# Performance work log

Hardware: AMD Instinct MI355X
Metric: run time of the kernel (lower is better)

## Reference

```python
import jax, jax.numpy as jnp
import numpy as np

DIM = 1024
NUM_HEADS = 16
HEAD_DIM = DIM // NUM_HEADS
CHUNK = 128
SCALE = HEAD_DIM ** -0.5
RMS_EPS_BIT = 1.1920929e-07  # torch.finfo(float32).eps (nn.RMSNorm default)
RMS_EPS_OUT = 1e-6


def activation_quant(x):
    scale = 127.0 / jnp.clip(jnp.max(jnp.abs(x), axis=-1, keepdims=True), 1e-5)
    return jnp.clip(jnp.round(x * scale), -128, 127) / scale


def weight_quant(w):
    scale = 1.0 / jnp.clip(jnp.mean(jnp.abs(w)), 1e-5)
    return jnp.clip(jnp.round(w * scale), -1, 1) / scale


def bitlinear(x, w, b, norm_w):
    xn = x * jax.lax.rsqrt(jnp.mean(x * x, axis=-1, keepdims=True) + RMS_EPS_BIT) * norm_w
    xq = xn + jax.lax.stop_gradient(activation_quant(xn) - xn)
    wq = w + jax.lax.stop_gradient(weight_quant(w) - w)
    return xq @ wq.T + b


def rms_norm(x, w):
    return x * jax.lax.rsqrt(jnp.mean(x * x, axis=-1, keepdims=True) + RMS_EPS_OUT) * w


def apply_rope(x, cos, sin):
    # x: [B,N,H,D]; cos/sin: [N, D//2]
    B, N, H, D = x.shape
    cos_e = jnp.repeat(cos[:N], 2, axis=-1)[None, :, None, :]  # [1,N,1,D]
    sin_e = jnp.repeat(sin[:N], 2, axis=-1)[None, :, None, :]
    xh = x.reshape(B, N, H, D // 2, 2)
    x_rot = jnp.stack([-xh[..., 1], xh[..., 0]], axis=-1).reshape(B, N, H, D)
    return x * cos_e + x_rot * sin_e


def setup_inputs() -> dict:
    key = jax.random.key(0)
    ks = jax.random.split(key, 8)
    B, N = 2, 8192
    return {
        "x": jax.random.normal(ks[0], (B, N, DIM), jnp.float32),
        "cos": jax.random.uniform(ks[1], (N, HEAD_DIM // 2), jnp.float32),
        "sin": jax.random.uniform(ks[2], (N, HEAD_DIM // 2), jnp.float32),
        "qkv_w": jax.random.normal(ks[3], (3 * DIM, DIM), jnp.float32) * 0.02,
        "qkv_b": jnp.zeros((3 * DIM,), jnp.float32),
        "qkv_nw": jnp.ones((DIM,), jnp.float32),
        "proj_w": jax.random.normal(ks[4], (DIM, DIM), jnp.float32) * 0.02,
        "proj_b": jnp.zeros((DIM,), jnp.float32),
        "proj_nw": jnp.ones((DIM,), jnp.float32),
        "norm_w": jnp.ones((DIM,), jnp.float32),
    }


def lightning_attention(x, cos, sin, qkv_w, qkv_b, qkv_nw, proj_w, proj_b, proj_nw, norm_w):
    B, N, C = x.shape
    qkv = bitlinear(x, qkv_w, qkv_b, qkv_nw).reshape(B, N, 3, NUM_HEADS, HEAD_DIM)
    q, k, v = qkv[:, :, 0], qkv[:, :, 1], qkv[:, :, 2]
    q = apply_rope(q, cos, sin)
    k = apply_rope(k, cos, sin)
    # N chosen as a multiple of CHUNK (pad_len == 0)
    T = N // CHUNK
    # [T, B, chunk, H, Dh]
    qc = jnp.moveaxis(q.reshape(B, T, CHUNK, NUM_HEADS, HEAD_DIM), 1, 0)
    kc = jnp.moveaxis(k.reshape(B, T, CHUNK, NUM_HEADS, HEAD_DIM), 1, 0)
    vc = jnp.moveaxis(v.reshape(B, T, CHUNK, NUM_HEADS, HEAD_DIM), 1, 0)
    causal = jnp.tril(jnp.ones((CHUNK, CHUNK), bool))
    neg_inf = jnp.finfo(x.dtype).min

    def step(kv_state, chunk):
        q_t, k_t, v_t = chunk  # each [B, chunk, H, Dh]
        scores = jnp.einsum('bqhd,bkhd->bhqk', q_t, k_t) * SCALE
        scores = jnp.where(causal, scores, neg_inf)
        attn = jax.nn.softmax(scores, axis=-1)
        o_intra = jnp.einsum('bhqk,bkhd->bqhd', attn, v_t)
        o_inter = jnp.einsum('bqhd,bhde->bqhe', q_t, kv_state)
        kv_new = kv_state + jnp.einsum('bkhd,bkhe->bhde', k_t, v_t)
        return kv_new, o_intra + o_inter

    kv0 = jnp.zeros((B, NUM_HEADS, HEAD_DIM, HEAD_DIM), x.dtype)
    _, out = jax.lax.scan(step, kv0, (qc, kc, vc))  # out: [T,B,chunk,H,Dh]
    out = jnp.moveaxis(out, 0, 1).reshape(B, N, C)
    return bitlinear(rms_norm(out, norm_w), proj_w, proj_b, proj_nw)


def reference(x, cos, sin, qkv_w, qkv_b, qkv_nw, proj_w, proj_b, proj_nw, norm_w):
    return lightning_attention(x, cos, sin, qkv_w, qkv_b, qkv_nw, proj_w, proj_b, proj_nw, norm_w)
```

## Files before the change

kernel.cpp:

```cpp
#include <hip/hip_runtime.h>


typedef unsigned short USH;
typedef __attribute__((ext_vector_type(8))) short short8;
typedef __attribute__((ext_vector_type(4))) float f32x4;
typedef __attribute__((ext_vector_type(4))) USH us4;

__device__ __forceinline__ float b2f(USH u) { return __uint_as_float(((unsigned)u) << 16); }
__device__ __forceinline__ USH f2b(float f) {
    unsigned u = __float_as_uint(f);
    u += 0x7fffu + ((u >> 16) & 1u);
    return (USH)(u >> 16);
}
__device__ __forceinline__ f32x4 mfma16(short8 a, short8 b, f32x4 c) {
    return __builtin_amdgcn_mfma_f32_16x16x32_bf16(a, b, c, 0, 0, 0);
}
__device__ __forceinline__ void gload_lds16(const void* g, void* l) {
    __builtin_amdgcn_global_load_lds(
        (const __attribute__((address_space(1))) unsigned*)g,
        (__attribute__((address_space(3))) unsigned*)l, 16, 0, 0);
}

__device__ __forceinline__ float blk_sum(float v, float* red) {
#pragma unroll
    for (int o = 32; o; o >>= 1) v += __shfl_xor(v, o);
    __syncthreads();
    if ((threadIdx.x & 63) == 0) red[threadIdx.x >> 6] = v;
    __syncthreads();
    return red[0] + red[1] + red[2] + red[3];
}
__device__ __forceinline__ float blk_max(float v, float* red) {
#pragma unroll
    for (int o = 32; o; o >>= 1) v = fmaxf(v, __shfl_xor(v, o));
    __syncthreads();
    if ((threadIdx.x & 63) == 0) red[threadIdx.x >> 6] = v;
    __syncthreads();
    return fmaxf(fmaxf(red[0], red[1]), fmaxf(red[2], red[3]));
}

__global__ __launch_bounds__(256) void k_wabs(const float* __restrict__ qw,
                                              const float* __restrict__ pw,
                                              float* __restrict__ partials) {
    __shared__ float red[4];
    int which = blockIdx.y;
    const float4* p = (const float4*)(which ? pw : qw);
    int n4 = which ? (1024 * 1024 / 4) : (3072 * 1024 / 4);
    float s = 0.f;
    for (int i = blockIdx.x * 256 + threadIdx.x; i < n4; i += 256 * 256) {
        float4 v = p[i];
        s += fabsf(v.x) + fabsf(v.y) + fabsf(v.z) + fabsf(v.w);
    }
#pragma unroll
    for (int o = 32; o; o >>= 1) s += __shfl_xor(s, o);
    if ((threadIdx.x & 63) == 0) red[threadIdx.x >> 6] = s;
    __syncthreads();
    if (threadIdx.x == 0)
        partials[which * 256 + blockIdx.x] = red[0] + red[1] + red[2] + red[3];
}

__global__ __launch_bounds__(256) void k_wsum(const float* __restrict__ partials,
                                              float* __restrict__ sums) {
    __shared__ double red[4];
    int which = blockIdx.x;
    double v = (double)partials[which * 256 + threadIdx.x];
#pragma unroll
    for (int o = 32; o; o >>= 1) v += __shfl_xor(v, o);
    if ((threadIdx.x & 63) == 0) red[threadIdx.x >> 6] = v;
    __syncthreads();
    if (threadIdx.x == 0)
        sums[which] = (float)(red[0] + red[1] + red[2] + red[3]);
}

__global__ __launch_bounds__(256) void k_wquant(const float* __restrict__ qw,
                                                const float* __restrict__ pw,
                                                const float* __restrict__ sums,
                                                USH* __restrict__ wqk, USH* __restrict__ wqp) {
    int id = blockIdx.x * 256 + threadIdx.x;
    float4 v; USH* dst; float sc;
    if (id < 786432) {
        v = ((const float4*)qw)[id];
        sc = 1.f / fmaxf(sums[0] * (1.f / 3145728.f), 1e-5f);
        dst = wqk + (size_t)id * 4;
    } else {
        int j = id - 786432;
        v = ((const float4*)pw)[j];
        sc = 1.f / fmaxf(sums[1] * (1.f / 1048576.f), 1e-5f);
        dst = wqp + (size_t)j * 4;
    }
    us4 o;
    o.x = f2b(fminf(fmaxf(rintf(v.x * sc), -1.f), 1.f));
    o.y = f2b(fminf(fmaxf(rintf(v.y * sc), -1.f), 1.f));
    o.z = f2b(fminf(fmaxf(rintf(v.z * sc), -1.f), 1.f));
    o.w = f2b(fminf(fmaxf(rintf(v.w * sc), -1.f), 1.f));
    *(us4*)dst = o;
}

__global__ __launch_bounds__(256) void k_actq(const float* __restrict__ x,
                                              const float* __restrict__ nw,
                                              USH* __restrict__ xq, float* __restrict__ inva) {
    __shared__ float red[4];
    int row = blockIdx.x, tid = threadIdx.x;
    float4 v = ((const float4*)(x + (size_t)row * 1024))[tid];
    float4 w = ((const float4*)nw)[tid];
    float ss = v.x * v.x + v.y * v.y + v.z * v.z + v.w * v.w;
    ss = blk_sum(ss, red);
    float r1 = rsqrtf(ss * (1.f / 1024.f) + 1.1920929e-07f);
    float x0 = v.x * r1 * w.x, x1 = v.y * r1 * w.y, x2 = v.z * r1 * w.z, x3 = v.w * r1 * w.w;
    float am = fmaxf(fmaxf(fabsf(x0), fabsf(x1)), fmaxf(fabsf(x2), fabsf(x3)));
    am = blk_max(am, red);
    float amc = fmaxf(am, 1e-5f);
    float sc = 127.f / amc;
    us4 o;
    o.x = f2b(fminf(fmaxf(rintf(x0 * sc), -128.f), 127.f));
    o.y = f2b(fminf(fmaxf(rintf(x1 * sc), -128.f), 127.f));
    o.z = f2b(fminf(fmaxf(rintf(x2 * sc), -128.f), 127.f));
    o.w = f2b(fminf(fmaxf(rintf(x3 * sc), -128.f), 127.f));
    *(us4*)(xq + (size_t)row * 1024 + tid * 4) = o;
    if (tid == 0) inva[row] = amc * (1.f / 127.f);
}

__global__ __launch_bounds__(256) void k_norm2q(const USH* __restrict__ oat,
                                                const float* __restrict__ nw,
                                                const float* __restrict__ pnw,
                                                USH* __restrict__ xq, float* __restrict__ inva) {
    __shared__ float red[4];
    int row = blockIdx.x, tid = threadIdx.x;
    us4 ov = *(const us4*)(oat + (size_t)row * 1024 + tid * 4);
    float o0 = b2f(ov.x), o1 = b2f(ov.y), o2 = b2f(ov.z), o3 = b2f(ov.w);
    float4 w = ((const float4*)nw)[tid];
    float4 pw = ((const float4*)pnw)[tid];
    float ss1 = blk_sum(o0 * o0 + o1 * o1 + o2 * o2 + o3 * o3, red);
    float r1 = rsqrtf(ss1 * (1.f / 1024.f) + 1e-6f);
    float y0 = o0 * r1 * w.x, y1 = o1 * r1 * w.y, y2 = o2 * r1 * w.z, y3 = o3 * r1 * w.w;
    float ss2 = blk_sum(y0 * y0 + y1 * y1 + y2 * y2 + y3 * y3, red);
    float r2 = rsqrtf(ss2 * (1.f / 1024.f) + 1.1920929e-07f);
    float z0 = y0 * r2 * pw.x, z1 = y1 * r2 * pw.y, z2 = y2 * r2 * pw.z, z3 = y3 * r2 * pw.w;
    float am = fmaxf(fmaxf(fabsf(z0), fabsf(z1)), fmaxf(fabsf(z2), fabsf(z3)));
    am = blk_max(am, red);
    float amc = fmaxf(am, 1e-5f);
    float sc = 127.f / amc;
    us4 q;
    q.x = f2b(fminf(fmaxf(rintf(z0 * sc), -128.f), 127.f));
    q.y = f2b(fminf(fmaxf(rintf(z1 * sc), -128.f), 127.f));
    q.z = f2b(fminf(fmaxf(rintf(z2 * sc), -128.f), 127.f));
    q.w = f2b(fminf(fmaxf(rintf(z3 * sc), -128.f), 127.f));
    *(us4*)(xq + (size_t)row * 1024 + tid * 4) = q;
    if (tid == 0) inva[row] = amc * (1.f / 127.f);
}

template <bool OUT_BF16>
__global__ __launch_bounds__(512, 2) void k_gemm(const USH* __restrict__ A, const USH* __restrict__ W,
                                                 const float* __restrict__ inva,
                                                 const float* __restrict__ wsum, float wcnt,
                                                 const float* __restrict__ bias,
                                                 void* __restrict__ out, int Nn, int K) {
    __shared__ __align__(16) USH lds[3 * 16384];
    const int tid = threadIdx.x;
    const int wv = tid >> 6, lane = tid & 63, quad = lane >> 4, lid = lane & 15;
    const int wr = wv >> 2, wc = wv & 3;

    const int nbn = gridDim.x;
    const int nwg = nbn * gridDim.y;
    const int bid = blockIdx.y * nbn + blockIdx.x;
    const int swb = (bid & 7) * (nwg >> 3) + (bid >> 3);
    const int bn = swb % nbn, bm = swb / nbn;

    const int T = K >> 5;

    const int r0s = wv * 16 + (lane >> 2);
    const int sw0 = (r0s & 3) ^ ((r0s >> 2) & 1);
    const int c0s = ((lane & 3) ^ sw0) * 8;
    const USH* ag0 = A + (size_t)(bm * 256 + r0s) * K + c0s;
    const USH* wg0 = W + (size_t)(bn * 256 + r0s) * K + c0s;
    const size_t J1 = (size_t)128 * K;

    const int sq = quad ^ ((lid & 3) ^ ((lid >> 2) & 1));
    const int arow = (wr * 128 + lid) * 32 + sq * 8;
    const int brow = (wc * 64 + lid) * 32 + sq * 8;

    f32x4 acc[8][4];
#pragma unroll
    for (int mt = 0; mt < 8; mt++)
#pragma unroll
        for (int nt = 0; nt < 4; nt++)
#pragma unroll
            for (int r = 0; r < 4; r++) acc[mt][nt][r] = 0.f;

#pragma unroll
    for (int t = 0; t < 3; t++) {
        USH* dst = &lds[t * 16384];
        gload_lds16(ag0 + t * 32,      &dst[wv * 512]);
        gload_lds16(ag0 + J1 + t * 32, &dst[(8 + wv) * 512]);
        gload_lds16(wg0 + t * 32,      &dst[8192 + wv * 512]);
        gload_lds16(wg0 + J1 + t * 32, &dst[8192 + (8 + wv) * 512]);
    }
    asm volatile("s_waitcnt vmcnt(8)" ::: "memory");
    __builtin_amdgcn_s_barrier();
    __builtin_amdgcn_sched_barrier(0);

    short8 afA[8], bfA[4], afB[8], bfB[4];
#pragma unroll
    for (int mt = 0; mt < 8; mt++) afA[mt] = *(const short8*)&lds[arow + mt * 512];
#pragma unroll
    for (int nt = 0; nt < 4; nt++) bfA[nt] = *(const short8*)&lds[8192 + brow + nt * 512];

#define GITER(t, afC, bfC, afN, bfN)                                              \
    do {                                                                          \
        const USH* Rd = &lds[(((t) + 1) % 3) * 16384];                            \
        USH* Sd = &lds[((t) % 3) * 16384];                                        \
        if ((t) + 2 < T) asm volatile("s_waitcnt vmcnt(4) lgkmcnt(0)" ::: "memory"); \
        else             asm volatile("s_waitcnt vmcnt(0) lgkmcnt(0)" ::: "memory"); \
        __builtin_amdgcn_s_barrier();                                             \
        __builtin_amdgcn_sched_barrier(0);                                        \
        if ((t) + 3 < T) {                                                        \
            gload_lds16(ag0 + ((t) + 3) * 32,      &Sd[wv * 512]);                \
            gload_lds16(ag0 + J1 + ((t) + 3) * 32, &Sd[(8 + wv) * 512]);          \
            gload_lds16(wg0 + ((t) + 3) * 32,      &Sd[8192 + wv * 512]);         \
            gload_lds16(wg0 + J1 + ((t) + 3) * 32, &Sd[8192 + (8 + wv) * 512]);   \
        }                                                                         \
        if ((t) + 1 < T) {                                                        \
            _Pragma("unroll")                                                     \
            for (int mt_ = 0; mt_ < 8; mt_++)                                     \
                afN[mt_] = *(const short8*)&Rd[arow + mt_ * 512];                 \
            _Pragma("unroll")                                                     \
            for (int nt_ = 0; nt_ < 4; nt_++)                                     \
                bfN[nt_] = *(const short8*)&Rd[8192 + brow + nt_ * 512];          \
        }                                                                         \
        __builtin_amdgcn_s_setprio(1);                                            \
        _Pragma("unroll")                                                         \
        for (int mt_ = 0; mt_ < 8; mt_++)                                         \
            _Pragma("unroll")                                                     \
            for (int nt_ = 0; nt_ < 4; nt_++)                                     \
                acc[mt_][nt_] = mfma16(afC[mt_], bfC[nt_], acc[mt_][nt_]);        \
        __builtin_amdgcn_s_setprio(0);                                            \
    } while (0)

    for (int tt = 0; tt < T; tt += 2) {
        GITER(tt,     afA, bfA, afB, bfB);
        GITER(tt + 1, afB, bfB, afA, bfA);
    }
#undef GITER

    float wm = fmaxf(wsum[0] * (1.f / wcnt), 1e-5f);
#pragma unroll
    for (int mt = 0; mt < 8; mt++)
#pragma unroll
        for (int r = 0; r < 4; r++) {
            int rowg = bm * 256 + wr * 128 + mt * 16 + quad * 4 + r;
            float ia = inva[rowg] * wm;
#pragma unroll
            for (int nt = 0; nt < 4; nt++) {
                int colg = bn * 256 + wc * 64 + nt * 16 + lid;
                float v = acc[mt][nt][r] * ia + bias[colg];
                if (OUT_BF16) ((USH*)out)[(size_t)rowg * Nn + colg] = f2b(v);
                else ((float*)out)[(size_t)rowg * Nn + colg] = v;
            }
        }
}

__global__ __launch_bounds__(256) void k_rope(USH* __restrict__ qkv,
                                              const float* __restrict__ cs,
                                              const float* __restrict__ sn) {
    int id = blockIdx.x * 256 + threadIdx.x;
    int rowm = id >> 8, p4 = id & 255;
    int part = p4 >> 7, pi = p4 & 127;
    int h = pi >> 3, i4 = pi & 7;
    int n = rowm & 8191;
    size_t a = (size_t)rowm * 3072 + part * 1024 + h * 64 + i4 * 8;
    short8 u = *(const short8*)(qkv + a);
    float4 c4 = *(const float4*)&cs[n * 32 + i4 * 4];
    float4 s4 = *(const float4*)&sn[n * 32 + i4 * 4];
    float c[4] = {c4.x, c4.y, c4.z, c4.w};
    float s[4] = {s4.x, s4.y, s4.z, s4.w};
    short8 y;
#pragma unroll
    for (int p = 0; p < 4; p++) {
        float x0 = b2f((USH)u[2 * p]);
        float x1 = b2f((USH)u[2 * p + 1]);
        y[2 * p]     = (short)f2b(x0 * c[p] - x1 * s[p]);
        y[2 * p + 1] = (short)f2b(x1 * c[p] + x0 * s[p]);
    }
    *(short8*)(qkv + a) = y;
}

__global__ __launch_bounds__(256) void k_attn_intra(const USH* __restrict__ qkv,
                                                    USH* __restrict__ oat,
                                                    float* __restrict__ kvc) {
    __shared__ char smem[36864 + 17408 + 17408];
    USH* qs = (USH*)smem;
    USH* kqs = qs + 128 * 72;
    USH* Ps = (USH*)smem;
    USH* vt = (USH*)(smem + 36864);
    USH* kt = (USH*)(smem + 36864 + 17408);
    int tid = threadIdx.x, wv = tid >> 6, lane = tid & 63, quad = lane >> 4, lid = lane & 15;
    int t = blockIdx.x, bh = blockIdx.y, b = bh >> 4, h = bh & 15;
    size_t base = ((size_t)(b * 8192 + t * 128)) * 3072 + h * 64;
    int r0 = tid >> 3, c0 = (tid & 7) * 8;
#pragma unroll
    for (int i = 0; i < 4; i++) {
        int r = i * 32 + r0;
        short8 qv = *(const short8*)(qkv + base + (size_t)r * 3072 + c0);
        short8 kv = *(const short8*)(qkv + base + (size_t)r * 3072 + 1024 + c0);
        short8 vv = *(const short8*)(qkv + base + (size_t)r * 3072 + 2048 + c0);
        *(short8*)&qs[r * 72 + c0] = qv;
        *(short8*)&kqs[r * 72 + c0] = kv;
        USH tmpv[8]; *(short8*)tmpv = vv;
        USH tmpk[8]; *(short8*)tmpk = kv;
#pragma unroll
        for (int j = 0; j < 8; j++) {
            vt[(c0 + j) * 136 + r] = tmpv[j];
            kt[(c0 + j) * 136 + r] = tmpk[j];
        }
    }
    __syncthreads();

    f32x4 accs[2][8];
#pragma unroll
    for (int mt = 0; mt < 2; mt++)
#pragma unroll
        for (int nt = 0; nt < 8; nt++)
#pragma unroll
            for (int r = 0; r < 4; r++) accs[mt][nt][r] = 0.f;
    int R = wv * 32;
#pragma unroll
    for (int ksx = 0; ksx < 2; ksx++) {
        int co = ksx * 32 + quad * 8;
        short8 af0 = *(const short8*)&qs[(R + lid) * 72 + co];
        short8 af1 = *(const short8*)&qs[(R + 16 + lid) * 72 + co];
        short8 bf[8];
#pragma unroll
        for (int nt = 0; nt < 8; nt++) bf[nt] = *(const short8*)&kqs[(nt * 16 + lid) * 72 + co];
#pragma unroll
        for (int nt = 0; nt < 8; nt++) {
            accs[0][nt] = mfma16(af0, bf[nt], accs[0][nt]);
            accs[1][nt] = mfma16(af1, bf[nt], accs[1][nt]);
        }
    }
#pragma unroll
    for (int mt = 0; mt < 2; mt++)
#pragma unroll
        for (int r = 0; r < 4; r++) {
            int row = R + mt * 16 + quad * 4 + r;
            float sv[8];
            float mx = -3.0e38f;
#pragma unroll
            for (int nt = 0; nt < 8; nt++) {
                int col = nt * 16 + lid;
                float v = accs[mt][nt][r] * 0.125f;
                sv[nt] = (col <= row) ? v : -3.0e38f;
                mx = fmaxf(mx, sv[nt]);
            }
#pragma unroll
            for (int o = 8; o; o >>= 1) mx = fmaxf(mx, __shfl_xor(mx, o));
            float sm = 0.f;
#pragma unroll
            for (int nt = 0; nt < 8; nt++) {
                float e = (sv[nt] > -1.0e38f) ? __expf(sv[nt] - mx) : 0.f;
                sv[nt] = e; sm += e;
            }
#pragma unroll
            for (int o = 8; o; o >>= 1) sm += __shfl_xor(sm, o);
            float inv = 1.f / sm;
#pragma unroll
            for (int nt = 0; nt < 8; nt++) accs[mt][nt][r] = sv[nt] * inv;
        }
    __syncthreads();
#pragma unroll
    for (int mt = 0; mt < 2; mt++)
#pragma unroll
        for (int nt = 0; nt < 8; nt++)
#pragma unroll
            for (int r = 0; r < 4; r++)
                Ps[(R + mt * 16 + quad * 4 + r) * 136 + nt * 16 + lid] = f2b(accs[mt][nt][r]);
    __syncthreads();

    f32x4 acco[8];
#pragma unroll
    for (int nt = 0; nt < 8; nt++)
#pragma unroll
        for (int r = 0; r < 4; r++) acco[nt][r] = 0.f;
#pragma unroll
    for (int kq = 0; kq < 4; kq++) {
        int co = kq * 32 + quad * 8;
        short8 av = *(const short8*)&vt[(wv * 16 + lid) * 136 + co];
#pragma unroll
        for (int nt = 0; nt < 8; nt++) {
            short8 bp = *(const short8*)&Ps[(nt * 16 + lid) * 136 + co];
            acco[nt] = mfma16(av, bp, acco[nt]);
        }
    }
    size_t obase = (size_t)(b * 8192 + t * 128) * 1024 + h * 64;
#pragma unroll
    for (int nt = 0; nt < 8; nt++)
#pragma unroll
        for (int r = 0; r < 4; r++) {
            int d = wv * 16 + quad * 4 + r;
            int q = nt * 16 + lid;
            oat[obase + (size_t)q * 1024 + d] = f2b(acco[nt][r]);
        }

    f32x4 acck[4];
#pragma unroll
    for (int nt = 0; nt < 4; nt++)
#pragma unroll
        for (int r = 0; r < 4; r++) acck[nt][r] = 0.f;
#pragma unroll
    for (int kq = 0; kq < 4; kq++) {
        int co = kq * 32 + quad * 8;
        short8 ak = *(const short8*)&kt[(wv * 16 + lid) * 136 + co];
#pragma unroll
        for (int nt = 0; nt < 4; nt++) {
            short8 bv = *(const short8*)&vt[(nt * 16 + lid) * 136 + co];
            acck[nt] = mfma16(ak, bv, acck[nt]);
        }
    }
    float* outk = kvc + ((size_t)bh * 64 + t) * 4096;
#pragma unroll
    for (int nt = 0; nt < 4; nt++)
#pragma unroll
        for (int r = 0; r < 4; r++) {
            int d = wv * 16 + quad * 4 + r, e = nt * 16 + lid;
            outk[d * 64 + e] = acck[nt][r];
        }
}

__global__ __launch_bounds__(256) void k_prefix(float* __restrict__ kvc) {
    int gid = blockIdx.x * 256 + threadIdx.x;
    int bh = gid >> 12, idx = gid & 4095;
    float* p = kvc + (size_t)bh * 64 * 4096 + idx;
    float a = 0.f;
    for (int t = 0; t < 64; t++) {
        float c = p[(size_t)t * 4096];
        p[(size_t)t * 4096] = a;
        a += c;
    }
}

__global__ __launch_bounds__(256) void k_ointer(const USH* __restrict__ qkv,
                                                const float* __restrict__ kvc,
                                                USH* __restrict__ oat) {
    __shared__ char smem[18432 + 9216];
    USH* qs = (USH*)smem;
    USH* kvt = (USH*)(smem + 18432);
    int tid = threadIdx.x, wv = tid >> 6, lane = tid & 63, quad = lane >> 4, lid = lane & 15;
    int t = blockIdx.x, bh = blockIdx.y, b = bh >> 4, h = bh & 15;
    size_t base = ((size_t)(b * 8192 + t * 128)) * 3072 + h * 64;
    int r0 = tid >> 3, c0 = (tid & 7) * 8;
#pragma unroll
    for (int i = 0; i < 4; i++) {
        int r = i * 32 + r0;
        short8 qv = *(const short8*)(qkv + base + (size_t)r * 3072 + c0);
        *(short8*)&qs[r * 72 + c0] = qv;
    }
    const float* kv = kvc + ((size_t)bh * 64 + t) * 4096;
#pragma unroll
    for (int j = 0; j < 16; j++) {
        int idx = j * 256 + tid;
        int d = idx >> 6, e = idx & 63;
        kvt[e * 72 + d] = f2b(kv[idx]);
    }
    __syncthreads();
    f32x4 acc[2][4];
#pragma unroll
    for (int mt = 0; mt < 2; mt++)
#pragma unroll
        for (int nt = 0; nt < 4; nt++)
#pragma unroll
            for (int r = 0; r < 4; r++) acc[mt][nt][r] = 0.f;
    int R = wv * 32;
#pragma unroll
    for (int kd = 0; kd < 2; kd++) {
        int co = kd * 32 + quad * 8;
        short8 a0 = *(const short8*)&qs[(R + lid) * 72 + co];
        short8 a1 = *(const short8*)&qs[(R + 16 + lid) * 72 + co];
#pragma unroll
        for (int nt = 0; nt < 4; nt++) {
            short8 bv = *(const short8*)&kvt[(nt * 16 + lid) * 72 + co];
            acc[0][nt] = mfma16(a0, bv, acc[0][nt]);
            acc[1][nt] = mfma16(a1, bv, acc[1][nt]);
        }
    }
#pragma unroll
    for (int mt = 0; mt < 2; mt++)
#pragma unroll
        for (int nt = 0; nt < 4; nt++)
#pragma unroll
            for (int r = 0; r < 4; r++) {
                int row = t * 128 + R + mt * 16 + quad * 4 + r;
                size_t idx = ((size_t)b * 8192 + row) * 1024 + h * 64 + nt * 16 + lid;
                float prev = b2f(oat[idx]);
                oat[idx] = f2b(prev + acc[mt][nt][r]);
            }
}

extern "C" void kernel_launch(void* const* d_in, const int* in_sizes, int n_in,
                              void* d_out, int out_size, void* d_ws, size_t ws_size,
                              hipStream_t stream) {
    const float* x      = (const float*)d_in[0];
    const float* cosp   = (const float*)d_in[1];
    const float* sinp   = (const float*)d_in[2];
    const float* qkv_w  = (const float*)d_in[3];
    const float* qkv_b  = (const float*)d_in[4];
    const float* qkv_nw = (const float*)d_in[5];
    const float* proj_w = (const float*)d_in[6];
    const float* proj_b = (const float*)d_in[7];
    const float* proj_nw= (const float*)d_in[8];
    const float* norm_w = (const float*)d_in[9];
    float* out = (float*)d_out;

    char* w = (char*)d_ws;
    float* sums    = (float*)(w + 0);
    float* partials= (float*)(w + 64);
    USH*   wq_qkv  = (USH*)(w + 4096);
    USH*   wq_proj = (USH*)(w + 4096 + 6291456);
    float* inva    = (float*)(w + 8392704);
    char*  R1      = w + 8458240;
    char*  R2      = w + 8458240 + 33554432;
    USH*   qkv     = (USH*)(w + 8458240 + 2ull * 33554432);
    USH*   xq      = (USH*)R1;
    USH*   oat     = (USH*)R1;
    float* kvc     = (float*)R2;
    USH*   xq2     = (USH*)R2;

    k_wabs<<<dim3(256, 2), 256, 0, stream>>>(qkv_w, proj_w, partials);
    k_wsum<<<2, 256, 0, stream>>>(partials, sums);
    k_wquant<<<4096, 256, 0, stream>>>(qkv_w, proj_w, sums, wq_qkv, wq_proj);
    k_actq<<<16384, 256, 0, stream>>>(x, qkv_nw, xq, inva);
    k_gemm<true><<<dim3(12, 64), 512, 0, stream>>>(xq, wq_qkv, inva, &sums[0], 3145728.f,
                                                   qkv_b, (void*)qkv, 3072, 1024);
    k_rope<<<16384, 256, 0, stream>>>(qkv, cosp, sinp);
    k_attn_intra<<<dim3(64, 32), 256, 0, stream>>>(qkv, oat, kvc);
    k_prefix<<<512, 256, 0, stream>>>(kvc);
    k_ointer<<<dim3(64, 32), 256, 0, stream>>>(qkv, kvc, oat);
    k_norm2q<<<16384, 256, 0, stream>>>(oat, norm_w, proj_nw, xq2, inva);
    k_gemm<false><<<dim3(4, 64), 512, 0, stream>>>(xq2, wq_proj, inva, &sums[1], 1048576.f,
                                                   proj_b, (void*)out, 1024, 1024);
    (void)in_sizes; (void)n_in; (void)out_size; (void)ws_size;
}
```

Baseline: 423.2 us.

## Switch GEMM to double-buffered LDS pipeline with higher occupancy bound

Replaces the triple-buffered LDS ring with register-fragment prefetch by a simpler double-buffered loop that waits for all outstanding loads each iteration, then loads fragments and runs the MFMAs. LDS use drops from 96KB to 64KB and launch bounds request 4 blocks per SM instead of 2, aiming to hide latency through occupancy rather than deep software pipelining. The catch is less in-block overlap: vmcnt(0) each step stalls on the prefetch, and with 128 accumulator floats per thread the register budget at the new bound may force spills.

```diff
diff --git a/kernel.cpp b/kernel.cpp
--- a/kernel.cpp
+++ b/kernel.cpp
@@ -149,12 +149,12 @@
 }
 
 template <bool OUT_BF16>
-__global__ __launch_bounds__(512, 2) void k_gemm(const USH* __restrict__ A, const USH* __restrict__ W,
+__global__ __launch_bounds__(512, 4) void k_gemm(const USH* __restrict__ A, const USH* __restrict__ W,
                                                  const float* __restrict__ inva,
                                                  const float* __restrict__ wsum, float wcnt,
                                                  const float* __restrict__ bias,
                                                  void* __restrict__ out, int Nn, int K) {
-    __shared__ __align__(16) USH lds[3 * 16384];
+    __shared__ __align__(16) USH lds[2 * 16384];
     const int tid = threadIdx.x;
     const int wv = tid >> 6, lane = tid & 63, quad = lane >> 4, lid = lane & 15;
     const int wr = wv >> 2, wc = wv & 3;
@@ -186,60 +186,38 @@
 #pragma unroll
             for (int r = 0; r < 4; r++) acc[mt][nt][r] = 0.f;
 
-#pragma unroll
-    for (int t = 0; t < 3; t++) {
-        USH* dst = &lds[t * 16384];
-        gload_lds16(ag0 + t * 32,      &dst[wv * 512]);
-        gload_lds16(ag0 + J1 + t * 32, &dst[(8 + wv) * 512]);
-        gload_lds16(wg0 + t * 32,      &dst[8192 + wv * 512]);
-        gload_lds16(wg0 + J1 + t * 32, &dst[8192 + (8 + wv) * 512]);
-    }
-    asm volatile("s_waitcnt vmcnt(8)" ::: "memory");
-    __builtin_amdgcn_s_barrier();
-    __builtin_amdgcn_sched_barrier(0);
-
-    short8 afA[8], bfA[4], afB[8], bfB[4];
-#pragma unroll
-    for (int mt = 0; mt < 8; mt++) afA[mt] = *(const short8*)&lds[arow + mt * 512];
-#pragma unroll
-    for (int nt = 0; nt < 4; nt++) bfA[nt] = *(const short8*)&lds[8192 + brow + nt * 512];
-
-#define GITER(t, afC, bfC, afN, bfN)                                              \
-    do {                                                                          \
-        const USH* Rd = &lds[(((t) + 1) % 3) * 16384];                            \
-        USH* Sd = &lds[((t) % 3) * 16384];                                        \
-        if ((t) + 2 < T) asm volatile("s_waitcnt vmcnt(4) lgkmcnt(0)" ::: "memory"); \
-        else             asm volatile("s_waitcnt vmcnt(0) lgkmcnt(0)" ::: "memory"); \
-        __builtin_amdgcn_s_barrier();                                             \
-        __builtin_amdgcn_sched_barrier(0);                                        \
-        if ((t) + 3 < T) {                                                        \
-            gload_lds16(ag0 + ((t) + 3) * 32,      &Sd[wv * 512]);                \
-            gload_lds16(ag0 + J1 + ((t) + 3) * 32, &Sd[(8 + wv) * 512]);          \
-            gload_lds16(wg0 + ((t) + 3) * 32,      &Sd[8192 + wv * 512]);         \
-            gload_lds16(wg0 + J1 + ((t) + 3) * 32, &Sd[8192 + (8 + wv) * 512]);   \
-        }                                                                         \
-        if ((t) + 1 < T) {                                                        \
-            _Pragma("unroll")                                                     \
-            for (int mt_ = 0; mt_ < 8; mt_++)                                     \
-                afN[mt_] = *(const short8*)&Rd[arow + mt_ * 512];                 \
-            _Pragma("unroll")                                                     \
-            for (int nt_ = 0; nt_ < 4; nt_++)                                     \
-                bfN[nt_] = *(const short8*)&Rd[8192 + brow + nt_ * 512];          \
-        }                                                                         \
-        __builtin_amdgcn_s_setprio(1);                                            \
-        _Pragma("unroll")                                                         \
-        for (int mt_ = 0; mt_ < 8; mt_++)                                         \
-            _Pragma("unroll")                                                     \
-            for (int nt_ = 0; nt_ < 4; nt_++)                                     \
-                acc[mt_][nt_] = mfma16(afC[mt_], bfC[nt_], acc[mt_][nt_]);        \
-        __builtin_amdgcn_s_setprio(0);                                            \
-    } while (0)
-
-    for (int tt = 0; tt < T; tt += 2) {
-        GITER(tt,     afA, bfA, afB, bfB);
-        GITER(tt + 1, afB, bfB, afA, bfA);
-    }
-#undef GITER
+    gload_lds16(ag0,      &lds[wv * 512]);
+    gload_lds16(ag0 + J1, &lds[(8 + wv) * 512]);
+    gload_lds16(wg0,      &lds[8192 + wv * 512]);
+    gload_lds16(wg0 + J1, &lds[8192 + (8 + wv) * 512]);
+
+    for (int t = 0; t < T; ++t) {
+        const USH* As = &lds[(t & 1) * 16384];
+        const USH* Bs = As + 8192;
+        USH* Pd = &lds[((t + 1) & 1) * 16384];
+        short8 af[8], bf[4];
+        asm volatile("s_waitcnt vmcnt(0) lgkmcnt(0)" ::: "memory");
+        __builtin_amdgcn_s_barrier();
+        __builtin_amdgcn_sched_barrier(0);
+        if (t + 1 < T) {
+            gload_lds16(ag0 + (t + 1) * 32,      &Pd[wv * 512]);
+            gload_lds16(ag0 + J1 + (t + 1) * 32, &Pd[(8 + wv) * 512]);
+            gload_lds16(wg0 + (t + 1) * 32,      &Pd[8192 + wv * 512]);
+            gload_lds16(wg0 + J1 + (t + 1) * 32, &Pd[8192 + (8 + wv) * 512]);
+        }
+#pragma unroll
+        for (int mt = 0; mt < 8; mt++)
+            af[mt] = *(const short8*)&As[arow + mt * 512];
+#pragma unroll
+        for (int nt = 0; nt < 4; nt++)
+            bf[nt] = *(const short8*)&Bs[brow + nt * 512];
+        __builtin_amdgcn_s_setprio(1);
+#pragma unroll
+        for (int mt = 0; mt < 8; mt++)
+#pragma unroll
+            for (int nt = 0; nt < 4; nt++) acc[mt][nt] = mfma16(af[mt], bf[nt], acc[mt][nt]);
+        __builtin_amdgcn_s_setprio(0);
+    }
 
     float wm = fmaxf(wsum[0] * (1.f / wcnt), 1e-5f);
 #pragma unroll
```

New measurement: 1.574 ms. 272% more time.
